# Kernel optimization log

Hardware: AMD Instinct MI355X
Metric: run time of the kernel (lower is better)

Reference implementation:

```python
import jax, jax.numpy as jnp
import numpy as np

N, D, E, TOP_K = 2048, 512, 16, 2
HID = 4 * D
EPS = 1e-10


def setup_inputs() -> dict:
    key = jax.random.key(0)
    ks = jax.random.split(key, 8)
    s = 0.02
    return {
        "x": jax.random.normal(ks[0], (N, D), dtype=jnp.float32),
        "w_norm": jnp.ones((D,), dtype=jnp.float32),
        "Wr": jax.random.normal(ks[1], (D, E), dtype=jnp.float32) * s,
        "br": jnp.zeros((E,), dtype=jnp.float32),
        "W1": jax.random.normal(ks[2], (E, D, HID), dtype=jnp.float32) * s,
        "b1": jnp.zeros((E, HID), dtype=jnp.float32),
        "W2": jax.random.normal(ks[3], (E, HID, D), dtype=jnp.float32) * s,
        "b2": jnp.zeros((E, D), dtype=jnp.float32),
    }


def reference(x, w_norm, Wr, br, W1, b1, W2, b2):
    res = x
    # RMSNorm over feature dim (dim=1 in the torch code for 2D input)
    rms = jnp.sqrt(jnp.mean(x * x, axis=1, keepdims=True) + EPS)
    xn = w_norm * (x / rms)
    # Router: top-k over expert logits, softmax over the k selected logits
    logits = xn @ Wr + br                      # [N, E]
    top_p, top_i = jax.lax.top_k(logits, TOP_K)  # [N, k]
    top_p = jax.nn.softmax(top_p, axis=-1)
    # Dense per-token expert weights [N, E] (top-k indices are distinct)
    weight = jnp.zeros((x.shape[0], E), dtype=x.dtype)
    weight = weight.at[jnp.arange(x.shape[0])[:, None], top_i].add(top_p)
    # All-expert FFN (dense reference for the routed dispatch)
    h = jnp.einsum("nd,edh->enh", xn, W1) + b1[:, None, :]   # [E, N, 4D]
    y = jnp.einsum("enh,ehd->end", jax.nn.silu(h), W2) + b2[:, None, :]  # [E, N, D]
    out = jnp.einsum("end,ne->nd", y, weight)
    return out + res
```

## Files before the change

### kernel.cpp

```cpp
#include <hip/hip_runtime.h>

#define N_TOK 2048
#define DIM   512
#define NEXP  16
#define HID   2048
#define NSLOT (N_TOK*2)

typedef __attribute__((ext_vector_type(8))) short short8;
typedef __attribute__((ext_vector_type(4))) float floatx4;

__device__ __forceinline__ ushort f2bf(float f) {
    union { float f; unsigned u; } c; c.f = f;
    unsigned u = c.u;
    unsigned r = (u + 0x7fffu + ((u >> 16) & 1u)) >> 16;
    return (ushort)r;
}
__device__ __forceinline__ float bf2f(ushort u) {
    union { unsigned u; float f; } c; c.u = ((unsigned)u) << 16;
    return c.f;
}

__device__ __forceinline__ void gl_lds16(const void* g, void* l) {
    __builtin_amdgcn_global_load_lds(
        (const __attribute__((address_space(1))) unsigned int*)g,
        (__attribute__((address_space(3))) unsigned int*)l, 16, 0, 0);
}

__device__ __forceinline__ void transpose_tile(const float* __restrict__ src,
                                               ushort* __restrict__ dst,
                                               int K, int Nn, int bx, void* smem)
{
    float* Ls = (float*)smem;
    const int NT = Nn >> 6;
    const int KT = K >> 6;
    const int nt = bx % NT; bx /= NT;
    const int kt = bx % KT; bx /= KT;
    const int e  = bx;
    const int t = threadIdx.x;

    const float* sp = src + ((size_t)e * K + kt * 64) * Nn + nt * 64;
#pragma unroll
    for (int i = 0; i < 4; i++) {
        const int k  = (t >> 4) + i * 16;
        const int c4 = (t & 15) * 4;
        const float4 v = *(const float4*)(sp + (size_t)k * Nn + c4);
        Ls[k * 65 + c4 + 0] = v.x;
        Ls[k * 65 + c4 + 1] = v.y;
        Ls[k * 65 + c4 + 2] = v.z;
        Ls[k * 65 + c4 + 3] = v.w;
    }
    __syncthreads();

    ushort* dp = dst + ((size_t)e * Nn + nt * 64) * K + kt * 64;
#pragma unroll
    for (int i = 0; i < 2; i++) {
        const int n = (t >> 3) + i * 32;
        const int c = t & 7;
        unsigned w[4];
#pragma unroll
        for (int q = 0; q < 4; q++) {
            const unsigned lo = f2bf(Ls[(c * 8 + q * 2 + 0) * 65 + n]);
            const unsigned hi = f2bf(Ls[(c * 8 + q * 2 + 1) * 65 + n]);
            w[q] = lo | (hi << 16);
        }
        uint4 o = make_uint4(w[0], w[1], w[2], w[3]);
        *(uint4*)(dp + (size_t)n * K + c * 8) = o;
    }
}

__global__ __launch_bounds__(256)
void router_fused(const float* __restrict__ x, const float* __restrict__ w_norm,
                  const float* __restrict__ Wr, const float* __restrict__ br,
                  ushort* __restrict__ xn, int2* __restrict__ rec_e,
                  float2* __restrict__ rec_w)
{
    __shared__ float xs[16][516];
    __shared__ float wrT[16][516];

    const int tid  = threadIdx.x;
    const int wave = tid >> 6, lane = tid & 63;
    const int tblk = blockIdx.x * 16;

#pragma unroll
    for (int k = 0; k < 32; k++) {
        const int idx = tid + k * 256;
        wrT[idx & 15][idx >> 4] = Wr[idx];
    }

    const float4* wnp = (const float4*)w_norm;
    const float4 wa = wnp[lane], wb = wnp[lane + 64];
#pragma unroll
    for (int i = 0; i < 4; i++) {
        const int tl = wave * 4 + i, t = tblk + tl;
        const float4* xp = (const float4*)(x + (size_t)t * DIM);
        const float4 a = xp[lane], b = xp[lane + 64];
        float ss = a.x*a.x + a.y*a.y + a.z*a.z + a.w*a.w
                 + b.x*b.x + b.y*b.y + b.z*b.z + b.w*b.w;
#pragma unroll
        for (int m = 32; m >= 1; m >>= 1) ss += __shfl_xor(ss, m, 64);
        const float rinv = 1.f / sqrtf(ss * (1.f / (float)DIM) + 1e-10f);
        float4 na, nb;
        na.x = a.x * wa.x * rinv; na.y = a.y * wa.y * rinv;
        na.z = a.z * wa.z * rinv; na.w = a.w * wa.w * rinv;
        nb.x = b.x * wb.x * rinv; nb.y = b.y * wb.y * rinv;
        nb.z = b.z * wb.z * rinv; nb.w = b.w * wb.w * rinv;
        *(float4*)&xs[tl][lane * 4]       = na;
        *(float4*)&xs[tl][256 + lane * 4] = nb;
        ushort4 ua, ub;
        ua.x = f2bf(na.x); ua.y = f2bf(na.y); ua.z = f2bf(na.z); ua.w = f2bf(na.w);
        ub.x = f2bf(nb.x); ub.y = f2bf(nb.y); ub.z = f2bf(nb.z); ub.w = f2bf(nb.w);
        ushort4* xo = (ushort4*)(xn + (size_t)t * DIM);
        xo[lane] = ua; xo[lane + 64] = ub;
    }
    __syncthreads();

    const int tl = tid >> 4, e = tid & 15;
    const int t = tblk + tl;
    float acc = 0.f;
#pragma unroll 4
    for (int d = 0; d < DIM; d += 4) {
        const float4 xv = *(const float4*)&xs[tl][d];
        const float4 wv = *(const float4*)&wrT[e][d];
        acc += xv.x * wv.x + xv.y * wv.y + xv.z * wv.z + xv.w * wv.w;
    }
    const float v = acc + br[e];

    float m0 = v; int i0 = e; float m1 = -1e30f; int i1 = 16;
#pragma unroll
    for (int msk = 1; msk < 16; msk <<= 1) {
        const float om0 = __shfl_xor(m0, msk, 64); const int oi0 = __shfl_xor(i0, msk, 64);
        const float om1 = __shfl_xor(m1, msk, 64); const int oi1 = __shfl_xor(i1, msk, 64);
        const bool bf_ = (om0 > m0) || (om0 == m0 && oi0 < i0);
        const float t0m = bf_ ? om0 : m0; const int t0i = bf_ ? oi0 : i0;
        const float l0m = bf_ ? m0 : om0; const int l0i = bf_ ? i0 : oi0;
        const bool b2_ = (om1 > m1) || (om1 == m1 && oi1 < i1);
        const float t2m = b2_ ? om1 : m1; const int t2i = b2_ ? oi1 : i1;
        const bool lw = (l0m > t2m) || (l0m == t2m && l0i < t2i);
        m0 = t0m; i0 = t0i;
        m1 = lw ? l0m : t2m; i1 = lw ? l0i : t2i;
    }
    if (e == 0) {
        const float ex = expf(m1 - m0);
        const float w0 = 1.f / (1.f + ex);
        rec_e[t] = make_int2(i0, i1);
        rec_w[t] = make_float2(w0, ex * w0);
    }
}

__global__ __launch_bounds__(1024)
void plan_kernel(const int2* __restrict__ rec_e, int* __restrict__ cnt,
                 int* __restrict__ off, int* __restrict__ tok_of_slot,
                 int* __restrict__ rec_slot)
{
    __shared__ int soff[17];
    const int e = threadIdx.x >> 6;
    const int lane = threadIdx.x & 63;

    int total = 0;
    for (int c = 0; c < N_TOK / 64; c++) {
        const int2 er = rec_e[c * 64 + lane];
        const bool hit = (er.x == e) || (er.y == e);
        total += __popcll(__ballot(hit));
    }
    if (lane == 0) soff[e + 1] = total;
    __syncthreads();
    if (threadIdx.x == 0) {
        soff[0] = 0;
        for (int q = 1; q <= 16; q++) soff[q] += soff[q - 1];
    }
    __syncthreads();
    int base = soff[e];
    if (lane == 0) { cnt[e] = soff[e + 1] - base; off[e] = base; }

    for (int c = 0; c < N_TOK / 64; c++) {
        const int t = c * 64 + lane;
        const int2 er = rec_e[t];
        const bool hit = (er.x == e) || (er.y == e);
        const unsigned long long b = __ballot(hit);
        if (hit) {
            const int slot = base + __popcll(b & ((1ull << lane) - 1ull));
            tok_of_slot[slot] = t;
            const int which = (er.y == e) ? 1 : 0;
            rec_slot[t * 2 + which] = slot;
        }
        base += __popcll(b);
    }
}

__global__ __launch_bounds__(256)
void gemm1_trw2(const ushort* __restrict__ A,
                const float* __restrict__ W1, const float* __restrict__ b1,
                const int* __restrict__ cnt, const int* __restrict__ off,
                const int* __restrict__ tok_of_slot,
                ushort* __restrict__ hout,
                const float* __restrict__ w2src, ushort* __restrict__ w2dst)
{
    __shared__ __align__(16) char smem[25088];

    if (blockIdx.y >= 64) {
        const int bx = (blockIdx.y - 64) * 32 + blockIdx.x;
        transpose_tile(w2src, w2dst, HID, DIM, bx, smem);
        return;
    }

    const int flat = blockIdx.x + (blockIdx.y << 5);
    const int x = flat & 7;
    const int g = flat >> 3;
    const int e  = x + ((g >> 7) << 3);
    const int r0_ = g & 127;
    const int nb = r0_ & 31, mt = r0_ >> 5;

    const int count = cnt[e];
    if (mt * 128 >= count) return;
    const int base = off[e];
    const int rows = min(128, count - mt * 128);
    const int n0   = nb * 64;

    ushort* As_ = (ushort*)smem;
    ushort* Bs_ = (ushort*)(smem + 16384);
    int*    toks = (int*)(smem + 24576);

    const int tid = threadIdx.x;
    if (tid < 128) {
        const int r = tid < rows ? tid : rows - 1;
        toks[tid] = tok_of_slot[base + mt * 128 + r];
    }
    __syncthreads();

    const int lane = tid & 63;
    const int wid  = tid >> 6;
    const int wm = wid >> 1, wn = wid & 1;
    const int fr = lane & 15, fg = lane >> 4;

    const int rl  = lane >> 2;
    const int sko = ((lane & 3) ^ ((lane >> 4) & 3)) * 8;

    const ushort* aptr[2];
#pragma unroll
    for (int j = 0; j < 2; j++) {
        const int s = wid * 2 + j;
        aptr[j] = A + (size_t)toks[s * 16 + rl] * DIM + sko;
    }
    const float* bsrc = W1 + ((size_t)e * DIM + wid * 8) * HID + n0 + lane;
    const int bwoff = lane * 32 + ((wid ^ ((lane >> 1) & 3)) * 8);

    float breg[8];
#define LOADB(ktn)                                                           \
    do {                                                                     \
        _Pragma("unroll")                                                    \
        for (int j = 0; j < 8; j++)                                          \
            breg[j] = bsrc[((size_t)(ktn) * 32 + j) * HID];                  \
    } while (0)
#define WRITEB(pb)                                                           \
    do {                                                                     \
        short8 bw;                                                           \
        _Pragma("unroll")                                                    \
        for (int j = 0; j < 8; j++) bw[j] = (short)f2bf(breg[j]);            \
        *(short8*)&Bs_[(pb) * 2048 + bwoff] = bw;                            \
    } while (0)
#define STAGEA(pb, k0)                                                       \
    do {                                                                     \
        _Pragma("unroll")                                                    \
        for (int j = 0; j < 2; j++)                                          \
            gl_lds16(aptr[j] + (k0), (void*)(&As_[(pb) * 4096 + (wid * 2 + j) * 512])); \
    } while (0)

    floatx4 acc[4][2];
#pragma unroll
    for (int mi = 0; mi < 4; mi++)
#pragma unroll
        for (int ni = 0; ni < 2; ni++)
#pragma unroll
            for (int r = 0; r < 4; r++) acc[mi][ni][r] = 0.f;

    STAGEA(0, 0);
    LOADB(0);
    asm volatile("s_waitcnt vmcnt(0)" ::: "memory");
    WRITEB(0);

    int cur = 0;
    const int cxor = (fr >> 2) & 3;
    const int cxb  = (fr >> 1) & 3;
    for (int kt = 0; kt < 16; kt++) {
        if (kt < 15) {
            LOADB(kt + 1);
            STAGEA(cur ^ 1, (kt + 1) * 32);
            asm volatile("s_waitcnt vmcnt(10) lgkmcnt(0)" ::: "memory");
        } else {
            asm volatile("s_waitcnt vmcnt(0) lgkmcnt(0)" ::: "memory");
        }
        __builtin_amdgcn_s_barrier();
        __builtin_amdgcn_sched_barrier(0);

        __builtin_amdgcn_s_setprio(1);
        {
            const int co = (fg ^ cxor) * 8;
            const int cob = (fg ^ cxb) * 8;
            short8 af[4], bfr[2];
#pragma unroll
            for (int mi = 0; mi < 4; mi++)
                af[mi] = *(const short8*)&As_[cur * 4096 + (wm * 64 + mi * 16 + fr) * 32 + co];
#pragma unroll
            for (int ni = 0; ni < 2; ni++)
                bfr[ni] = *(const short8*)&Bs_[cur * 2048 + (wn * 32 + ni * 16 + fr) * 32 + cob];
#pragma unroll
            for (int mi = 0; mi < 4; mi++)
#pragma unroll
                for (int ni = 0; ni < 2; ni++)
                    acc[mi][ni] = __builtin_amdgcn_mfma_f32_16x16x32_bf16(af[mi], bfr[ni], acc[mi][ni], 0, 0, 0);
        }
        __builtin_amdgcn_s_setprio(0);

        __builtin_amdgcn_sched_barrier(0);
        __builtin_amdgcn_s_barrier();

        if (kt < 15) {
            asm volatile("s_waitcnt vmcnt(2)" ::: "memory");
            WRITEB(cur ^ 1);
        }
        cur ^= 1;
    }
#undef LOADB
#undef WRITEB
#undef STAGEA

#pragma unroll
    for (int ni = 0; ni < 2; ni++) {
        const int gn = n0 + wn * 32 + ni * 16 + fr;
        const float bv = b1[e * HID + gn];
#pragma unroll
        for (int mi = 0; mi < 4; mi++) {
#pragma unroll
            for (int r = 0; r < 4; r++) {
                const int lm = wm * 64 + mi * 16 + fg * 4 + r;
                if (lm < rows) {
                    const int slot = base + mt * 128 + lm;
                    float v = acc[mi][ni][r] + bv;
                    v = v / (1.f + __expf(-v));
                    hout[(size_t)slot * HID + gn] = f2bf(v);
                }
            }
        }
    }
}

__global__ __launch_bounds__(256)
void gemm2_kernel(const ushort* __restrict__ A,
                  const ushort* __restrict__ WT,
                  const int* __restrict__ cnt, const int* __restrict__ off,
                  ushort* __restrict__ yout)
{
    const int flat = blockIdx.x + (blockIdx.y << 5);
    const int x = flat & 7;
    const int g = flat >> 3;
    const int G = ((g >> 5) << 3) + x;
    const int e = G >> 2, z = G & 3;
    const int idx = g & 31;
    const int mt = idx >> 3, nb = idx & 7;

    const int count = cnt[e];
    if (mt * 128 >= count) return;
    const int base = off[e];
    const int rows = min(128, count - mt * 128);
    const int n0   = nb * 64;
    const int kbeg = z * 512;
    ushort* yp = yout + (size_t)z * NSLOT * DIM;

    __shared__ __align__(16) ushort As[2][128 * 32];
    __shared__ __align__(16) ushort Bs[2][64 * 32];
    __shared__ int toks[128];

    const int tid = threadIdx.x;
    if (tid < 128) {
        const int r = tid < rows ? tid : rows - 1;
        toks[tid] = base + mt * 128 + r;
    }
    __syncthreads();

    const int lane = tid & 63;
    const int wid  = tid >> 6;
    const int wm = wid >> 1, wn = wid & 1;
    const int fr = lane & 15, fg = lane >> 4;

    const int rl  = lane >> 2;
    const int sko = ((lane & 3) ^ ((lane >> 4) & 3)) * 8;

    const ushort* aptr[2];
#pragma unroll
    for (int j = 0; j < 2; j++) {
        const int s = wid * 2 + j;
        aptr[j] = A + (size_t)toks[s * 16 + rl] * HID + kbeg + sko;
    }
    const ushort* bptr = WT + ((size_t)e * DIM + n0 + wid * 16 + rl) * HID + kbeg + sko;

    floatx4 acc[4][2];
#pragma unroll
    for (int mi = 0; mi < 4; mi++)
#pragma unroll
        for (int ni = 0; ni < 2; ni++)
#pragma unroll
            for (int r = 0; r < 4; r++) acc[mi][ni][r] = 0.f;

#define STAGE2(pb, k0)                                                       \
    do {                                                                     \
        _Pragma("unroll")                                                    \
        for (int j = 0; j < 2; j++)                                          \
            gl_lds16(aptr[j] + (k0), (void*)(&As[pb][(wid * 2 + j) * 512])); \
        gl_lds16(bptr + (k0), (void*)(&Bs[pb][wid * 512]));                  \
    } while (0)

    int cur = 0;
    STAGE2(0, 0);

    const int cxor = (fr >> 2) & 3;
    for (int kt = 0; kt < 16; kt++) {
        if (kt < 15) {
            STAGE2(cur ^ 1, (kt + 1) * 32);
            asm volatile("s_waitcnt vmcnt(3)" ::: "memory");
        } else {
            asm volatile("s_waitcnt vmcnt(0)" ::: "memory");
        }
        __builtin_amdgcn_s_barrier();
        __builtin_amdgcn_sched_barrier(0);

        __builtin_amdgcn_s_setprio(1);
        {
            const int co = (fg ^ cxor) * 8;
            short8 af[4], bfr[2];
#pragma unroll
            for (int mi = 0; mi < 4; mi++)
                af[mi] = *(const short8*)&As[cur][(wm * 64 + mi * 16 + fr) * 32 + co];
#pragma unroll
            for (int ni = 0; ni < 2; ni++)
                bfr[ni] = *(const short8*)&Bs[cur][(wn * 32 + ni * 16 + fr) * 32 + co];
#pragma unroll
            for (int mi = 0; mi < 4; mi++)
#pragma unroll
                for (int ni = 0; ni < 2; ni++)
                    acc[mi][ni] = __builtin_amdgcn_mfma_f32_16x16x32_bf16(af[mi], bfr[ni], acc[mi][ni], 0, 0, 0);
        }
        __builtin_amdgcn_s_setprio(0);

        __builtin_amdgcn_sched_barrier(0);
        __builtin_amdgcn_s_barrier();
        cur ^= 1;
    }
#undef STAGE2

#pragma unroll
    for (int ni = 0; ni < 2; ni++) {
        const int gn = n0 + wn * 32 + ni * 16 + fr;
#pragma unroll
        for (int mi = 0; mi < 4; mi++) {
#pragma unroll
            for (int r = 0; r < 4; r++) {
                const int lm = wm * 64 + mi * 16 + fg * 4 + r;
                if (lm < rows) {
                    const int slot = base + mt * 128 + lm;
                    yp[(size_t)slot * DIM + gn] = f2bf(acc[mi][ni][r]);
                }
            }
        }
    }
}

__global__ __launch_bounds__(128)
void gather_kernel(const float* __restrict__ x, const ushort* __restrict__ ypart,
                   const float* __restrict__ b2,
                   const int2* __restrict__ rec_e, const float2* __restrict__ rec_w,
                   const int2* __restrict__ rec_slot, float* __restrict__ out)
{
    const int t = blockIdx.x;
    const int d4 = threadIdx.x * 4;
    const int2 ei = rec_e[t];
    const float2 w = rec_w[t];
    const int2 sl = rec_slot[t];
    const float4 xv  = *(const float4*)(x  + (size_t)t * DIM + d4);
    float4 s0 = make_float4(0.f, 0.f, 0.f, 0.f);
    float4 s1 = make_float4(0.f, 0.f, 0.f, 0.f);
#pragma unroll
    for (int kc = 0; kc < 4; kc++) {
        const ushort* yp = ypart + (size_t)kc * NSLOT * DIM;
        const ushort4 a = *(const ushort4*)(yp + (size_t)sl.x * DIM + d4);
        const ushort4 b = *(const ushort4*)(yp + (size_t)sl.y * DIM + d4);
        s0.x += bf2f(a.x); s0.y += bf2f(a.y); s0.z += bf2f(a.z); s0.w += bf2f(a.w);
        s1.x += bf2f(b.x); s1.y += bf2f(b.y); s1.z += bf2f(b.z); s1.w += bf2f(b.w);
    }
    const float4 b0  = *(const float4*)(b2 + (size_t)ei.x * DIM + d4);
    const float4 b1v = *(const float4*)(b2 + (size_t)ei.y * DIM + d4);
    float4 o;
    o.x = xv.x + w.x * (s0.x + b0.x) + w.y * (s1.x + b1v.x);
    o.y = xv.y + w.x * (s0.y + b0.y) + w.y * (s1.y + b1v.y);
    o.z = xv.z + w.x * (s0.z + b0.z) + w.y * (s1.z + b1v.z);
    o.w = xv.w + w.x * (s0.w + b0.w) + w.y * (s1.w + b1v.w);
    *(float4*)(out + (size_t)t * DIM + d4) = o;
}

extern "C" void kernel_launch(void* const* d_in, const int* in_sizes, int n_in,
                              void* d_out, int out_size, void* d_ws, size_t ws_size,
                              hipStream_t stream)
{
    const float* x  = (const float*)d_in[0];
    const float* wn = (const float*)d_in[1];
    const float* Wr = (const float*)d_in[2];
    const float* br = (const float*)d_in[3];
    const float* W1 = (const float*)d_in[4];
    const float* b1 = (const float*)d_in[5];
    const float* W2 = (const float*)d_in[6];
    const float* b2 = (const float*)d_in[7];
    float* out = (float*)d_out;

    char* ws = (char*)d_ws;
    ushort* W2T   = (ushort*)(ws);
    ushort* xn    = (ushort*)(ws + (32u << 20));
    ushort* h_buf = (ushort*)(ws + (34u << 20));
    ushort* y_par = (ushort*)(ws + (50u << 20));
    char* p = ws + (80u << 20);
    int*    cnt         = (int*)p;    p += 256;
    int*    off         = (int*)p;    p += 256;
    int2*   rec_e       = (int2*)p;   p += N_TOK * 8;
    float2* rec_w       = (float2*)p; p += N_TOK * 8;
    int2*   rec_slot    = (int2*)p;   p += N_TOK * 8;
    int*    tok_of_slot = (int*)p;    p += NSLOT * 4;

    router_fused<<<N_TOK / 16, 256, 0, stream>>>(x, wn, Wr, br, xn, rec_e, rec_w);

    plan_kernel<<<1, 1024, 0, stream>>>(rec_e, cnt, off, tok_of_slot, (int*)rec_slot);

    gemm1_trw2<<<dim3(32, 192), 256, 0, stream>>>(
        xn, W1, b1, cnt, off, tok_of_slot, h_buf, W2, W2T);

    gemm2_kernel<<<dim3(32, 64), 256, 0, stream>>>(h_buf, W2T, cnt, off, y_par);

    gather_kernel<<<N_TOK, 128, 0, stream>>>(x, y_par, b2, rec_e, rec_w, rec_slot, out);
}
```

Before: 96.97 us.

## Fuse W2 fp32-to-bf16 conversion into gemm2 B-tile loading, drop transpose pass

Removes the separate W2 transpose/convert blocks that ran alongside gemm1. gemm2 now loads fp32 W2 directly with register loads, converts to bf16, and writes swizzled tiles into LDS inside its double-buffered loop. This avoids writing and rereading a bf16 W2T copy, but gemm2 now reads fp32 weights with strided scalar loads and adds conversion work and extra waits inside the K loop. Only experts with routed tokens touch their W2 slices, so weights for idle tiles are no longer converted.

```diff
diff --git a/kernel.cpp b/kernel.cpp
--- a/kernel.cpp
+++ b/kernel.cpp
@@ -24,48 +24,6 @@
     __builtin_amdgcn_global_load_lds(
         (const __attribute__((address_space(1))) unsigned int*)g,
         (__attribute__((address_space(3))) unsigned int*)l, 16, 0, 0);
-}
-
-__device__ __forceinline__ void transpose_tile(const float* __restrict__ src,
-                                               ushort* __restrict__ dst,
-                                               int K, int Nn, int bx, void* smem)
-{
-    float* Ls = (float*)smem;
-    const int NT = Nn >> 6;
-    const int KT = K >> 6;
-    const int nt = bx % NT; bx /= NT;
-    const int kt = bx % KT; bx /= KT;
-    const int e  = bx;
-    const int t = threadIdx.x;
-
-    const float* sp = src + ((size_t)e * K + kt * 64) * Nn + nt * 64;
-#pragma unroll
-    for (int i = 0; i < 4; i++) {
-        const int k  = (t >> 4) + i * 16;
-        const int c4 = (t & 15) * 4;
-        const float4 v = *(const float4*)(sp + (size_t)k * Nn + c4);
-        Ls[k * 65 + c4 + 0] = v.x;
-        Ls[k * 65 + c4 + 1] = v.y;
-        Ls[k * 65 + c4 + 2] = v.z;
-        Ls[k * 65 + c4 + 3] = v.w;
-    }
-    __syncthreads();
-
-    ushort* dp = dst + ((size_t)e * Nn + nt * 64) * K + kt * 64;
-#pragma unroll
-    for (int i = 0; i < 2; i++) {
-        const int n = (t >> 3) + i * 32;
-        const int c = t & 7;
-        unsigned w[4];
-#pragma unroll
-        for (int q = 0; q < 4; q++) {
-            const unsigned lo = f2bf(Ls[(c * 8 + q * 2 + 0) * 65 + n]);
-            const unsigned hi = f2bf(Ls[(c * 8 + q * 2 + 1) * 65 + n]);
-            w[q] = lo | (hi << 16);
-        }
-        uint4 o = make_uint4(w[0], w[1], w[2], w[3]);
-        *(uint4*)(dp + (size_t)n * K + c * 8) = o;
-    }
 }
 
 __global__ __launch_bounds__(256)
@@ -188,21 +146,12 @@
 }
 
 __global__ __launch_bounds__(256)
-void gemm1_trw2(const ushort* __restrict__ A,
-                const float* __restrict__ W1, const float* __restrict__ b1,
-                const int* __restrict__ cnt, const int* __restrict__ off,
-                const int* __restrict__ tok_of_slot,
-                ushort* __restrict__ hout,
-                const float* __restrict__ w2src, ushort* __restrict__ w2dst)
+void gemm1_kernel(const ushort* __restrict__ A,
+                  const float* __restrict__ W1, const float* __restrict__ b1,
+                  const int* __restrict__ cnt, const int* __restrict__ off,
+                  const int* __restrict__ tok_of_slot,
+                  ushort* __restrict__ hout)
 {
-    __shared__ __align__(16) char smem[25088];
-
-    if (blockIdx.y >= 64) {
-        const int bx = (blockIdx.y - 64) * 32 + blockIdx.x;
-        transpose_tile(w2src, w2dst, HID, DIM, bx, smem);
-        return;
-    }
-
     const int flat = blockIdx.x + (blockIdx.y << 5);
     const int x = flat & 7;
     const int g = flat >> 3;
@@ -216,9 +165,9 @@
     const int rows = min(128, count - mt * 128);
     const int n0   = nb * 64;
 
-    ushort* As_ = (ushort*)smem;
-    ushort* Bs_ = (ushort*)(smem + 16384);
-    int*    toks = (int*)(smem + 24576);
+    __shared__ __align__(16) ushort As_[2 * 4096];
+    __shared__ __align__(16) ushort Bs_[2 * 2048];
+    __shared__ int toks[128];
 
     const int tid = threadIdx.x;
     if (tid < 128) {
@@ -346,7 +295,7 @@
 
 __global__ __launch_bounds__(256)
 void gemm2_kernel(const ushort* __restrict__ A,
-                  const ushort* __restrict__ WT,
+                  const float* __restrict__ W2,
                   const int* __restrict__ cnt, const int* __restrict__ off,
                   ushort* __restrict__ yout)
 {
@@ -366,8 +315,8 @@
     const int kbeg = z * 512;
     ushort* yp = yout + (size_t)z * NSLOT * DIM;
 
-    __shared__ __align__(16) ushort As[2][128 * 32];
-    __shared__ __align__(16) ushort Bs[2][64 * 32];
+    __shared__ __align__(16) ushort As_[2 * 4096];
+    __shared__ __align__(16) ushort Bs_[2 * 2048];
     __shared__ int toks[128];
 
     const int tid = threadIdx.x;
@@ -391,34 +340,53 @@
         const int s = wid * 2 + j;
         aptr[j] = A + (size_t)toks[s * 16 + rl] * HID + kbeg + sko;
     }
-    const ushort* bptr = WT + ((size_t)e * DIM + n0 + wid * 16 + rl) * HID + kbeg + sko;
-
-    floatx4 acc[4][2];
-#pragma unroll
-    for (int mi = 0; mi < 4; mi++)
-#pragma unroll
-        for (int ni = 0; ni < 2; ni++)
-#pragma unroll
-            for (int r = 0; r < 4; r++) acc[mi][ni][r] = 0.f;
-
-#define STAGE2(pb, k0)                                                       \
+    const float* bsrc = W2 + ((size_t)e * HID + kbeg + wid * 8) * DIM + n0 + lane;
+    const int bwoff = lane * 32 + ((wid ^ ((lane >> 1) & 3)) * 8);
+
+    float breg[8];
+#define LOADB(ktn)                                                           \
+    do {                                                                     \
+        _Pragma("unroll")                                                    \
+        for (int j = 0; j < 8; j++)                                          \
+            breg[j] = bsrc[((size_t)(ktn) * 32 + j) * DIM];                  \
+    } while (0)
+#define WRITEB(pb)                                                           \
+    do {                                                                     \
+        short8 bw;                                                           \
+        _Pragma("unroll")                                                    \
+        for (int j = 0; j < 8; j++) bw[j] = (short)f2bf(breg[j]);            \
+        *(short8*)&Bs_[(pb) * 2048 + bwoff] = bw;                            \
+    } while (0)
+#define STAGEA(pb, k0)                                                       \
     do {                                                                     \
         _Pragma("unroll")                                                    \
         for (int j = 0; j < 2; j++)                                          \
-            gl_lds16(aptr[j] + (k0), (void*)(&As[pb][(wid * 2 + j) * 512])); \
-        gl_lds16(bptr + (k0), (void*)(&Bs[pb][wid * 512]));                  \
+            gl_lds16(aptr[j] + (k0), (void*)(&As_[(pb) * 4096 + (wid * 2 + j) * 512])); \
     } while (0)
 
+    floatx4 acc[4][2];
+#pragma unroll
+    for (int mi = 0; mi < 4; mi++)
+#pragma unroll
+        for (int ni = 0; ni < 2; ni++)
+#pragma unroll
+            for (int r = 0; r < 4; r++) acc[mi][ni][r] = 0.f;
+
+    STAGEA(0, 0);
+    LOADB(0);
+    asm volatile("s_waitcnt vmcnt(0)" ::: "memory");
+    WRITEB(0);
+
     int cur = 0;
-    STAGE2(0, 0);
-
     const int cxor = (fr >> 2) & 3;
+    const int cxb  = (fr >> 1) & 3;
     for (int kt = 0; kt < 16; kt++) {
         if (kt < 15) {
-            STAGE2(cur ^ 1, (kt + 1) * 32);
-            asm volatile("s_waitcnt vmcnt(3)" ::: "memory");
+            LOADB(kt + 1);
+            STAGEA(cur ^ 1, (kt + 1) * 32);
+            asm volatile("s_waitcnt vmcnt(10) lgkmcnt(0)" ::: "memory");
         } else {
-            asm volatile("s_waitcnt vmcnt(0)" ::: "memory");
+            asm volatile("s_waitcnt vmcnt(0) lgkmcnt(0)" ::: "memory");
         }
         __builtin_amdgcn_s_barrier();
         __builtin_amdgcn_sched_barrier(0);
@@ -426,13 +394,14 @@
         __builtin_amdgcn_s_setprio(1);
         {
             const int co = (fg ^ cxor) * 8;
+            const int cob = (fg ^ cxb) * 8;
             short8 af[4], bfr[2];
 #pragma unroll
             for (int mi = 0; mi < 4; mi++)
-                af[mi] = *(const short8*)&As[cur][(wm * 64 + mi * 16 + fr) * 32 + co];
+                af[mi] = *(const short8*)&As_[cur * 4096 + (wm * 64 + mi * 16 + fr) * 32 + co];
 #pragma unroll
             for (int ni = 0; ni < 2; ni++)
-                bfr[ni] = *(const short8*)&Bs[cur][(wn * 32 + ni * 16 + fr) * 32 + co];
+                bfr[ni] = *(const short8*)&Bs_[cur * 2048 + (wn * 32 + ni * 16 + fr) * 32 + cob];
 #pragma unroll
             for (int mi = 0; mi < 4; mi++)
 #pragma unroll
@@ -443,9 +412,16 @@
 
         __builtin_amdgcn_sched_barrier(0);
         __builtin_amdgcn_s_barrier();
+
+        if (kt < 15) {
+            asm volatile("s_waitcnt vmcnt(2)" ::: "memory");
+            WRITEB(cur ^ 1);
+        }
         cur ^= 1;
     }
-#undef STAGE2
+#undef LOADB
+#undef WRITEB
+#undef STAGEA
 
 #pragma unroll
     for (int ni = 0; ni < 2; ni++) {
@@ -511,11 +487,10 @@
     float* out = (float*)d_out;
 
     char* ws = (char*)d_ws;
-    ushort* W2T   = (ushort*)(ws);
-    ushort* xn    = (ushort*)(ws + (32u << 20));
-    ushort* h_buf = (ushort*)(ws + (34u << 20));
-    ushort* y_par = (ushort*)(ws + (50u << 20));
-    char* p = ws + (80u << 20);
+    ushort* xn    = (ushort*)(ws);
+    ushort* h_buf = (ushort*)(ws + (2u  << 20));
+    ushort* y_par = (ushort*)(ws + (18u << 20));
+    char* p = ws + (40u << 20);
     int*    cnt         = (int*)p;    p += 256;
     int*    off         = (int*)p;    p += 256;
     int2*   rec_e       = (int2*)p;   p += N_TOK * 8;
@@ -527,10 +502,10 @@
 
     plan_kernel<<<1, 1024, 0, stream>>>(rec_e, cnt, off, tok_of_slot, (int*)rec_slot);
 
-    gemm1_trw2<<<dim3(32, 192), 256, 0, stream>>>(
-        xn, W1, b1, cnt, off, tok_of_slot, h_buf, W2, W2T);
-
-    gemm2_kernel<<<dim3(32, 64), 256, 0, stream>>>(h_buf, W2T, cnt, off, y_par);
+    gemm1_kernel<<<dim3(32, 64), 256, 0, stream>>>(
+        xn, W1, b1, cnt, off, tok_of_slot, h_buf);
+
+    gemm2_kernel<<<dim3(32, 64), 256, 0, stream>>>(h_buf, W2, cnt, off, y_par);
 
     gather_kernel<<<N_TOK, 128, 0, stream>>>(x, y_par, b2, rec_e, rec_w, rec_slot, out);
 }
```

After: 96.27 us, median of 2. Within noise of the previous version (-0.7%).
